# Optimization experiments

Hardware: AMD Instinct MI355X
Metric: run time of the kernel (lower is better)

## Reference

```python
import jax, jax.numpy as jnp
import numpy as np

B, M, DM = 8, 1024, 1024
H, DH, R = 16, 64, 32
DFF, R1, R2, RO = 4096, 512, 512, 512
EPS = 1e-12


def layernorm(x, g, b):
    mu = jnp.mean(x, axis=-1, keepdims=True)
    var = jnp.mean(jnp.square(x - mu), axis=-1, keepdims=True)
    return (x - mu) * jax.lax.rsqrt(var + EPS) * g + b


def setup_inputs() -> dict:
    key = jax.random.key(0)
    ks = jax.random.split(key, 24)
    s = lambda *sh: 1.0 / np.sqrt(sh[-2] if len(sh) > 1 else sh[-1])
    d = {}
    d['x'] = jax.random.normal(ks[0], (B, M, DM), jnp.float32)
    d['mask'] = jnp.zeros((B, M), jnp.float32)  # additive attention mask
    # per-head low-rank QKV factors: P:(H,DM,R), V:(H,R,DH), b:(H,DH)
    for i, nm in enumerate(['q', 'k', 'v']):
        d['P' + nm] = jax.random.normal(ks[1 + 3 * i], (H, DM, R), jnp.float32) * 0.02
        d['V' + nm] = jax.random.normal(ks[2 + 3 * i], (H, R, DH), jnp.float32) * 0.02
        d['b' + nm] = jnp.zeros((H, DH), jnp.float32)
    # attention output projection (low-rank) + LN1
    d['Uo'] = jax.random.normal(ks[10], (DM, RO), jnp.float32) * 0.02
    d['Vo'] = jax.random.normal(ks[11], (RO, DM), jnp.float32) * 0.02
    d['bo_attn'] = jnp.zeros((DM,), jnp.float32)
    d['g1'] = jnp.ones((DM,), jnp.float32)
    d['beta1'] = jnp.zeros((DM,), jnp.float32)
    # FFN low-rank factors + LN2
    d['U1'] = jax.random.normal(ks[12], (DM, R1), jnp.float32) * 0.02
    d['V1'] = jax.random.normal(ks[13], (R1, DFF), jnp.float32) * 0.02
    d['b1'] = jnp.zeros((DFF,), jnp.float32)
    d['U2'] = jax.random.normal(ks[14], (DFF, R2), jnp.float32) * 0.02
    d['V2'] = jax.random.normal(ks[15], (R2, DM), jnp.float32) * 0.02
    d['b2'] = jnp.zeros((DM,), jnp.float32)
    d['g2'] = jnp.ones((DM,), jnp.float32)
    d['beta2'] = jnp.zeros((DM,), jnp.float32)
    return d


def reference(x, mask, Pq, Vq, bq, Pk, Vk, bk, Pv, Vv, bv,
              Uo, Vo, bo_attn, g1, beta1,
              U1, V1, b1, U2, V2, b2, g2, beta2):
    # low-rank Q/K/V: x @ P -> (B,H,M,R), then @ V -> (B,H,M,DH), + bias
    def qkv(P, V, b):
        tmp = jnp.einsum('bmd,hdr->bhmr', x, P)
        return jnp.einsum('bhmr,hre->bhme', tmp, V) + b[None, :, None, :]

    Q = qkv(Pq, Vq, bq)
    K = qkv(Pk, Vk, bk)
    V = qkv(Pv, Vv, bv)
    scale = 1.0 / jnp.sqrt(jnp.asarray(DH, x.dtype))
    scores = jnp.einsum('bhme,bhne->bhmn', Q, K) * scale
    scores = scores + mask[:, None, None, :]  # additive mask broadcast over heads/queries
    probs = jax.nn.softmax(scores, axis=-1)
    attn = jnp.einsum('bhmn,bhne->bhme', probs, V)  # (B,H,M,DH)
    attn = attn.transpose(0, 2, 1, 3).reshape(attn.shape[0], attn.shape[2], -1)  # (B,M,DM)
    x1 = layernorm(x + (attn @ Uo) @ Vo + bo_attn, g1, beta1)
    # FFN: GELU((x1 @ U1) @ V1 + b1) @ U2 @ V2 + b2 (flashsvd_ffn semantics)
    mid = x1 @ U1
    hidden = jax.nn.gelu(mid @ V1 + b1, approximate=False)
    y = (hidden @ U2) @ V2 + b2
    return layernorm(x1 + y, g2, beta2)
```

## Files before the change

### kernel.cpp

```cpp
#include <hip/hip_runtime.h>
#include <hip/hip_bf16.h>
#include <math.h>

typedef unsigned short u16;
typedef unsigned int u32;
typedef __attribute__((ext_vector_type(8))) short bf16x8;
typedef __attribute__((ext_vector_type(4))) float f32x4;
typedef __attribute__((ext_vector_type(2))) unsigned int u32x2;
typedef __attribute__((ext_vector_type(4))) unsigned int u32x4;

#define B_ 8
#define M_ 1024
#define DM_ 1024
#define H_ 16
#define DH_ 64
#define NR_ 8192

__device__ __forceinline__ u16 f2bf(float f) {
    unsigned u = __float_as_uint(f);
    u += 0x7FFFu + ((u >> 16) & 1u);
    return (u16)(u >> 16);
}

__device__ __forceinline__ void gload16(const void* g, void* l) {
    __builtin_amdgcn_global_load_lds(
        (const __attribute__((address_space(1))) void*)g,
        (__attribute__((address_space(3))) void*)l, 16, 0, 0);
}

__device__ __forceinline__ u32 lds_addr(const void* p) {
    return (u32)(uintptr_t)(const __attribute__((address_space(3))) void*)p;
}

__device__ void conv_dev(const float* __restrict__ in, u16* __restrict__ out,
                         int bid, int tid) {
#pragma unroll
    for (int j = 0; j < 4; ++j) {
        int i = bid * 4096 + j * 1024 + tid * 4;
        float4 v = *reinterpret_cast<const float4*>(in + i);
        unsigned long long p = (unsigned long long)f2bf(v.x)
                             | ((unsigned long long)f2bf(v.y) << 16)
                             | ((unsigned long long)f2bf(v.z) << 32)
                             | ((unsigned long long)f2bf(v.w) << 48);
        *reinterpret_cast<unsigned long long*>(out + i) = p;
    }
}

__device__ void prep_p_dev(const float* __restrict__ P, u16* __restrict__ Pt,
                           int h, int kc, int tid, float* sm) {
    float (*Ps)[33] = (float(*)[33])sm;
#pragma unroll
    for (int i = 0; i < 16; ++i) {
        int e = tid + i * 256;
        int kk = e >> 5, r = e & 31;
        Ps[kk][r] = P[(size_t)h * 32768 + (size_t)(kc + kk) * 32 + r];
    }
    __syncthreads();
#pragma unroll
    for (int i = 0; i < 16; ++i) {
        int e = tid + i * 256;
        int r = e >> 7, k = e & 127;
        Pt[(size_t)(h * 32 + r) * 1024 + kc + k] = f2bf(Ps[k][r]);
    }
}

__device__ void prep_f_dev(const float* __restrict__ V, u16* __restrict__ Ft,
                           int h, int tid, float* sm) {
    float (*Vs)[65] = (float(*)[65])sm;
#pragma unroll
    for (int i = 0; i < 8; ++i) {
        int e = tid + i * 256;
        int r = e >> 6, c = e & 63;
        Vs[r][c] = V[(size_t)h * 2048 + r * 64 + c];
    }
    __syncthreads();
#pragma unroll
    for (int i = 0; i < 8; ++i) {
        int idx = tid + i * 256;
        int e = idx >> 5, r = idx & 31;
        Ft[(size_t)h * 2560 + e * 40 + r] = f2bf(Vs[r][e]);
    }
}

__device__ void transp_dev(const float* __restrict__ in, u16* __restrict__ out,
                           int R, int C, int bx, int by, int tid, float* sm) {
    float (*t)[65] = (float(*)[65])sm;
    const int rb = by * 64, cb = bx * 64;
#pragma unroll
    for (int i = 0; i < 16; ++i) {
        int e = tid + i * 256;
        int r = e >> 6, c = e & 63;
        t[r][c] = in[(size_t)(rb + r) * C + cb + c];
    }
    __syncthreads();
#pragma unroll
    for (int i = 0; i < 16; ++i) {
        int e = tid + i * 256;
        int r = e >> 6, c = e & 63;
        out[(size_t)(cb + r) * R + rb + c] = f2bf(t[c][r]);
    }
}

__global__ __launch_bounds__(256) void prep_all(
    const float* __restrict__ x,
    const float* __restrict__ Pq, const float* __restrict__ Pk, const float* __restrict__ Pv,
    const float* __restrict__ Vq, const float* __restrict__ Vk, const float* __restrict__ Vv,
    const float* __restrict__ Uo, const float* __restrict__ Vo,
    const float* __restrict__ U1, const float* __restrict__ V1,
    const float* __restrict__ U2, const float* __restrict__ V2,
    u16* __restrict__ Xb, u16* __restrict__ Pt,
    u16* __restrict__ Ftq, u16* __restrict__ Ftk, u16* __restrict__ Ftv,
    u16* __restrict__ Uot, u16* __restrict__ Vot,
    u16* __restrict__ U1t, u16* __restrict__ V1t,
    u16* __restrict__ U2t, u16* __restrict__ V2t) {
    __shared__ float smem[4224];
    const int bid = blockIdx.x, tid = threadIdx.x;
    if (bid < 2048) {
        conv_dev(x, Xb, bid, tid);
    } else if (bid < 2432) {
        int t = bid - 2048, which = t >> 7, tt = t & 127;
        const float* P = which == 0 ? Pq : (which == 1 ? Pk : Pv);
        prep_p_dev(P, Pt + (size_t)which * 524288, tt >> 3, (tt & 7) * 128, tid, smem);
    } else if (bid < 2480) {
        int t = bid - 2432, which = t >> 4;
        const float* V = which == 0 ? Vq : (which == 1 ? Vk : Vv);
        u16* F = which == 0 ? Ftq : (which == 1 ? Ftk : Ftv);
        prep_f_dev(V, F, t & 15, tid, smem);
    } else if (bid < 2608) {
        int t = bid - 2480;
        transp_dev(Uo, Uot, 1024, 512, t & 7, t >> 3, tid, smem);
    } else if (bid < 2736) {
        int t = bid - 2608;
        transp_dev(Vo, Vot, 512, 1024, t & 15, t >> 4, tid, smem);
    } else if (bid < 2864) {
        int t = bid - 2736;
        transp_dev(U1, U1t, 1024, 512, t & 7, t >> 3, tid, smem);
    } else if (bid < 3376) {
        int t = bid - 2864;
        transp_dev(V1, V1t, 512, 4096, t & 63, t >> 6, tid, smem);
    } else if (bid < 3888) {
        int t = bid - 3376;
        transp_dev(U2, U2t, 4096, 512, t & 7, t >> 3, tid, smem);
    } else {
        int t = bid - 3888;
        transp_dev(V2, V2t, 512, 1024, t & 15, t >> 4, tid, smem);
    }
}

template <int EPI, int NF>
__global__ __launch_bounds__(256) void gemm_bf16(const u16* __restrict__ A,
                                                 const u16* __restrict__ Bt,
                                                 const float* __restrict__ bias,
                                                 void* __restrict__ Cout,
                                                 int K, int N) {
    constexpr int BN = NF * 32;
    __shared__ u16 As[128 * 64];
    __shared__ u16 Bs[BN * 64];
    const int tid = threadIdx.x;
    const int lane = tid & 63, wv = tid >> 6;

    const int NX = gridDim.x;
    const int flat = blockIdx.x + blockIdx.y * NX;
    const int q = (NX * gridDim.y) >> 3;
    const int nid = (flat & 7) * q + (flat >> 3);
    const int row0 = (nid / NX) * 128, col0 = (nid % NX) * BN;

    const int frow = lane & 15, fk8 = lane >> 4;
    const int wm = (wv >> 1) * 64, wn = (wv & 1) * (BN / 2);

    f32x4 acc[4][NF];
    const f32x4 z4 = {0.f, 0.f, 0.f, 0.f};
#pragma unroll
    for (int i = 0; i < 4; ++i)
#pragma unroll
        for (int j = 0; j < NF; ++j) acc[i][j] = z4;

    for (int k0 = 0; k0 < K; k0 += 64) {
#pragma unroll
        for (int i = 0; i < 4; ++i) {
            int rr = (i * 4 + wv) * 8 + (lane >> 3);
            int cc = ((lane & 7) ^ (rr & 7)) * 8;
            gload16(A + (size_t)(row0 + rr) * K + k0 + cc,
                    (char*)As + (i * 4 + wv) * 1024);
        }
#pragma unroll
        for (int i = 0; i < NF; ++i) {
            int rr = (i * 4 + wv) * 8 + (lane >> 3);
            int cc = ((lane & 7) ^ (rr & 7)) * 8;
            gload16(Bt + (size_t)(col0 + rr) * K + k0 + cc,
                    (char*)Bs + (i * 4 + wv) * 1024);
        }
        asm volatile("s_waitcnt vmcnt(0)" ::: "memory");
        __syncthreads();
#pragma unroll
        for (int kf = 0; kf < 2; ++kf) {
            bf16x8 af[4], bfr[NF];
#pragma unroll
            for (int mf = 0; mf < 4; ++mf) {
                int r = wm + mf * 16 + frow;
                int c16 = (kf * 4 + fk8) ^ (r & 7);
                af[mf] = *reinterpret_cast<const bf16x8*>((char*)As + r * 128 + c16 * 16);
            }
#pragma unroll
            for (int nf = 0; nf < NF; ++nf) {
                int r = wn + nf * 16 + frow;
                int c16 = (kf * 4 + fk8) ^ (r & 7);
                bfr[nf] = *reinterpret_cast<const bf16x8*>((char*)Bs + r * 128 + c16 * 16);
            }
#pragma unroll
            for (int mf = 0; mf < 4; ++mf)
#pragma unroll
                for (int nf = 0; nf < NF; ++nf)
                    acc[mf][nf] = __builtin_amdgcn_mfma_f32_16x16x32_bf16(
                        af[mf], bfr[nf], acc[mf][nf], 0, 0, 0);
        }
        __syncthreads();
    }

    const int orow = fk8 * 4, ocol = frow;
#pragma unroll
    for (int mf = 0; mf < 4; ++mf)
#pragma unroll
        for (int nf = 0; nf < NF; ++nf)
#pragma unroll
            for (int j = 0; j < 4; ++j) {
                int row = row0 + wm + mf * 16 + orow + j;
                int col = col0 + wn + nf * 16 + ocol;
                float v = acc[mf][nf][j];
                if (EPI == 2) {
                    v += bias[col];
                    v = 0.5f * v * (1.f + erff(v * 0.70710678118f));
                    ((u16*)Cout)[(size_t)row * N + col] = f2bf(v);
                } else if (EPI == 3) {
                    ((float*)Cout)[(size_t)row * N + col] = v;
                } else {
                    ((u16*)Cout)[(size_t)row * N + col] = f2bf(v);
                }
            }
}

__global__ __launch_bounds__(256) void gemm_db(const u16* __restrict__ A,
                                               const u16* __restrict__ Bt,
                                               u16* __restrict__ Cout,
                                               int K, int N) {
    __shared__ u16 As[2][128 * 64];
    __shared__ u16 Bs[2][64 * 64];
    const int tid = threadIdx.x;
    const int lane = tid & 63, wv = tid >> 6;

    const int NX = gridDim.x;
    const int flat = blockIdx.x + blockIdx.y * NX;
    const int q = (NX * gridDim.y) >> 3;
    const int nid = (flat & 7) * q + (flat >> 3);
    const int row0 = (nid / NX) * 128, col0 = (nid % NX) * 64;

    const int frow = lane & 15, fk8 = lane >> 4;
    const int wm = (wv >> 1) * 64, wn = (wv & 1) * 32;

    f32x4 acc[4][2];
    const f32x4 z4 = {0.f, 0.f, 0.f, 0.f};
#pragma unroll
    for (int i = 0; i < 4; ++i) {
        acc[i][0] = z4;
        acc[i][1] = z4;
    }

    const int srr = (lane >> 3);
    const int scc = (lane & 7);

#pragma unroll
    for (int i = 0; i < 4; ++i) {
        int rr = (i * 4 + wv) * 8 + srr;
        int cc = (scc ^ (rr & 7)) * 8;
        gload16(A + (size_t)(row0 + rr) * K + cc, (char*)&As[0][0] + (i * 4 + wv) * 1024);
    }
#pragma unroll
    for (int i = 0; i < 2; ++i) {
        int rr = (i * 4 + wv) * 8 + srr;
        int cc = (scc ^ (rr & 7)) * 8;
        gload16(Bt + (size_t)(col0 + rr) * K + cc, (char*)&Bs[0][0] + (i * 4 + wv) * 1024);
    }

    int cur = 0;
    for (int k0 = 0; k0 < K; k0 += 64) {
        __syncthreads();
        if (k0 + 64 < K) {
            int kn = k0 + 64;
#pragma unroll
            for (int i = 0; i < 4; ++i) {
                int rr = (i * 4 + wv) * 8 + srr;
                int cc = (scc ^ (rr & 7)) * 8;
                gload16(A + (size_t)(row0 + rr) * K + kn + cc,
                        (char*)&As[cur ^ 1][0] + (i * 4 + wv) * 1024);
            }
#pragma unroll
            for (int i = 0; i < 2; ++i) {
                int rr = (i * 4 + wv) * 8 + srr;
                int cc = (scc ^ (rr & 7)) * 8;
                gload16(Bt + (size_t)(col0 + rr) * K + kn + cc,
                        (char*)&Bs[cur ^ 1][0] + (i * 4 + wv) * 1024);
            }
        }
#pragma unroll
        for (int kf = 0; kf < 2; ++kf) {
            bf16x8 af[4], bfr[2];
#pragma unroll
            for (int mf = 0; mf < 4; ++mf) {
                int r = wm + mf * 16 + frow;
                int c16 = (kf * 4 + fk8) ^ (r & 7);
                af[mf] = *reinterpret_cast<const bf16x8*>((char*)&As[cur][0] + r * 128 + c16 * 16);
            }
#pragma unroll
            for (int nf = 0; nf < 2; ++nf) {
                int r = wn + nf * 16 + frow;
                int c16 = (kf * 4 + fk8) ^ (r & 7);
                bfr[nf] = *reinterpret_cast<const bf16x8*>((char*)&Bs[cur][0] + r * 128 + c16 * 16);
            }
#pragma unroll
            for (int mf = 0; mf < 4; ++mf)
#pragma unroll
                for (int nf = 0; nf < 2; ++nf)
                    acc[mf][nf] = __builtin_amdgcn_mfma_f32_16x16x32_bf16(
                        af[mf], bfr[nf], acc[mf][nf], 0, 0, 0);
        }
        cur ^= 1;
    }

#pragma unroll
    for (int mf = 0; mf < 4; ++mf)
#pragma unroll
        for (int nf = 0; nf < 2; ++nf)
#pragma unroll
            for (int j = 0; j < 4; ++j) {
                int row = row0 + wm + mf * 16 + fk8 * 4 + j;
                int col = col0 + wn + nf * 16 + frow;
                Cout[(size_t)row * N + col] = f2bf(acc[mf][nf][j]);
            }
}

__global__ __launch_bounds__(256) void qkv_s2(const u16* __restrict__ Tmp,
                                              const u16* __restrict__ Ftq,
                                              const u16* __restrict__ Ftk,
                                              const u16* __restrict__ Ftv,
                                              const float* __restrict__ bq,
                                              const float* __restrict__ bk,
                                              const float* __restrict__ bv,
                                              u16* __restrict__ Q,
                                              u16* __restrict__ K,
                                              u16* __restrict__ V) {
    __shared__ u16 Ts[64 * 104];
    const int m0 = blockIdx.x * 64, h = blockIdx.y, tid = threadIdx.x;
    const int lane = tid & 63, wv = tid >> 6;
    const int frow = lane & 15, fk8 = lane >> 4;

    {
        const int row = tid >> 2, seg = tid & 3;
#pragma unroll
        for (int sect = 0; sect < 3; ++sect) {
            int off = sect * 512 + h * 32;
            uint4 v = *reinterpret_cast<const uint4*>(
                Tmp + (size_t)(m0 + row) * 1536 + off + seg * 8);
            *reinterpret_cast<uint4*>(&Ts[row * 104 + sect * 32 + seg * 8]) = v;
        }
    }
    __syncthreads();

    const u16* Fts[3] = {Ftq, Ftk, Ftv};
    const float* bs[3] = {bq, bk, bv};
    u16* outs[3] = {Q, K, V};

    f32x4 acc[3][4];
    const f32x4 z4 = {0.f, 0.f, 0.f, 0.f};
#pragma unroll
    for (int f = 0; f < 3; ++f) {
        bf16x8 a = *reinterpret_cast<const bf16x8*>(
            &Ts[(wv * 16 + frow) * 104 + f * 32 + fk8 * 8]);
#pragma unroll
        for (int nf = 0; nf < 4; ++nf) {
            int e = nf * 16 + frow;
            bf16x8 b = *reinterpret_cast<const bf16x8*>(
                Fts[f] + (size_t)h * 2560 + e * 40 + fk8 * 8);
            acc[f][nf] = __builtin_amdgcn_mfma_f32_16x16x32_bf16(a, b, z4, 0, 0, 0);
        }
    }

    const int bb = m0 >> 10;
#pragma unroll
    for (int f = 0; f < 3; ++f)
#pragma unroll
        for (int nf = 0; nf < 4; ++nf) {
            int e = nf * 16 + frow;
            float bias = bs[f][h * 64 + e];
#pragma unroll
            for (int j = 0; j < 4; ++j) {
                int m = m0 + wv * 16 + fk8 * 4 + j;
                outs[f][(((size_t)(bb * 16 + h) << 10) + (m & 1023)) * 64 + e] =
                    f2bf(acc[f][nf][j] + bias);
            }
        }
}

__global__ __launch_bounds__(256) void attn_mfma(const u16* __restrict__ Q,
                                                 const u16* __restrict__ K,
                                                 const u16* __restrict__ V,
                                                 const float* __restrict__ mask,
                                                 u16* __restrict__ O) {
    __shared__ u16 Ks[4096];
    __shared__ u16 Vt[4096];
    __shared__ u16 Pw[4096];
    const int flat = blockIdx.x;
    const int nid = (flat & 7) * 256 + (flat >> 3);
    const int hb = nid >> 4, qt = nid & 15;
    const int b = hb >> 4, h = hb & 15;
    const int tid = threadIdx.x, lane = tid & 63, wv = tid >> 6;
    const int frow = lane & 15, fk8 = lane >> 4;
    const size_t base = (size_t)hb * 65536;
    const float LOG2E = 1.44269504089f;
    const int srr = lane >> 3, scc = lane & 7;

#pragma unroll
    for (int i = 0; i < 2; ++i) {
        int rr = (i * 4 + wv) * 8 + srr;
        int cc = (scc ^ (rr & 7)) * 8;
        gload16(Q + base + (size_t)(qt * 64 + rr) * 64 + cc,
                (char*)Ks + (i * 4 + wv) * 1024);
    }
    asm volatile("s_waitcnt vmcnt(0)" ::: "memory");
    __syncthreads();
    bf16x8 qfrag[2];
#pragma unroll
    for (int kf = 0; kf < 2; ++kf) {
        int qr = wv * 16 + frow;
        int c16 = (kf * 4 + fk8) ^ (qr & 7);
        qfrag[kf] = *reinterpret_cast<const bf16x8*>((char*)Ks + qr * 128 + c16 * 16);
    }

    int voff[2];
#pragma unroll
    for (int i = 0; i < 2; ++i) {
        int c = (i * 4 + wv) * 64 + lane;
        int kb = c >> 5, db = (c >> 3) & 3, kr = (c >> 1) & 3, hf = c & 1;
        voff[i] = (kb * 4 + kr) * 64 + db * 16 + hf * 8;
    }

    u32 vta[4];
    {
        u32 vt0 = lds_addr(Vt) + fk8 * 1024 + frow * 2;
#pragma unroll
        for (int nf = 0; nf < 4; ++nf) vta[nf] = vt0 + nf * 128;
    }

    char* pwW = (char*)Pw + wv * 2048 + frow * 128 + (fk8 & 1) * 8;
    char* pwR = (char*)Pw + wv * 2048 + frow * 128;
    const float* mrow = mask + b * M_;

    float m_i = -1e30f, l_i = 0.f;
    const f32x4 z4 = {0.f, 0.f, 0.f, 0.f};
    f32x4 o_acc[4] = {z4, z4, z4, z4};

    for (int kt = 0; kt < 16; ++kt) {
        __syncthreads();
#pragma unroll
        for (int i = 0; i < 2; ++i) {
            int rr = (i * 4 + wv) * 8 + srr;
            int cc = (scc ^ (rr & 7)) * 8;
            gload16(K + base + (size_t)(kt * 64 + rr) * 64 + cc,
                    (char*)Ks + (i * 4 + wv) * 1024);
        }
#pragma unroll
        for (int i = 0; i < 2; ++i)
            gload16(V + base + kt * 4096 + voff[i], (char*)Vt + (i * 4 + wv) * 1024);
        asm volatile("s_waitcnt vmcnt(0)" ::: "memory");
        __syncthreads();

        f32x4 sacc[4] = {z4, z4, z4, z4};
        __builtin_amdgcn_s_setprio(1);
#pragma unroll
        for (int kf = 0; kf < 2; ++kf)
#pragma unroll
            for (int nf = 0; nf < 4; ++nf) {
                int kr = nf * 16 + frow;
                int c16 = (kf * 4 + fk8) ^ (kr & 7);
                bf16x8 ak = *reinterpret_cast<const bf16x8*>((char*)Ks + kr * 128 + c16 * 16);
                sacc[nf] = __builtin_amdgcn_mfma_f32_16x16x32_bf16(ak, qfrag[kf], sacc[nf], 0, 0, 0);
            }
        __builtin_amdgcn_s_setprio(0);

        float tval[4][4];
        float tmax = -1e30f;
#pragma unroll
        for (int nf = 0; nf < 4; ++nf) {
            float4 mk = *reinterpret_cast<const float4*>(mrow + kt * 64 + nf * 16 + fk8 * 4);
            float t0 = fmaf(sacc[nf][0], 0.125f, mk.x);
            float t1 = fmaf(sacc[nf][1], 0.125f, mk.y);
            float t2 = fmaf(sacc[nf][2], 0.125f, mk.z);
            float t3 = fmaf(sacc[nf][3], 0.125f, mk.w);
            tval[nf][0] = t0; tval[nf][1] = t1; tval[nf][2] = t2; tval[nf][3] = t3;
            tmax = fmaxf(tmax, fmaxf(fmaxf(t0, t1), fmaxf(t2, t3)));
        }
        tmax = fmaxf(tmax, __shfl_xor(tmax, 16));
        tmax = fmaxf(tmax, __shfl_xor(tmax, 32));

        if (__any(tmax > m_i + 8.f)) {
            float mnew = fmaxf(m_i, tmax);
            float c = exp2f((m_i - mnew) * LOG2E);
            m_i = mnew;
            l_i *= c;
#pragma unroll
            for (int j = 0; j < 4; ++j) {
                float cj = __shfl(c, fk8 * 4 + j);
#pragma unroll
                for (int nf = 0; nf < 4; ++nf) o_acc[nf][j] *= cj;
            }
        }

        const float ml = m_i * LOG2E;
        float rs = 0.f;
#pragma unroll
        for (int nf = 0; nf < 4; ++nf) {
            float p0 = exp2f(fmaf(tval[nf][0], LOG2E, -ml));
            float p1 = exp2f(fmaf(tval[nf][1], LOG2E, -ml));
            float p2 = exp2f(fmaf(tval[nf][2], LOG2E, -ml));
            float p3 = exp2f(fmaf(tval[nf][3], LOG2E, -ml));
            rs += (p0 + p1) + (p2 + p3);
            u32 w0 = __builtin_amdgcn_perm(__float_as_uint(p1), __float_as_uint(p0), 0x07060302u);
            u32 w1 = __builtin_amdgcn_perm(__float_as_uint(p3), __float_as_uint(p2), 0x07060302u);
            u32x2 wp = {w0, w1};
            *reinterpret_cast<u32x2*>(pwW + (((nf * 2 + (fk8 >> 1)) ^ (frow & 7)) * 16)) = wp;
        }
        rs += __shfl_xor(rs, 16);
        rs += __shfl_xor(rs, 32);
        l_i += rs;

#pragma unroll
        for (int kf = 0; kf < 2; ++kf) {
            bf16x8 ap = *reinterpret_cast<const bf16x8*>(pwR + (((kf * 4 + fk8) ^ (frow & 7)) * 16));
            u32x2 r0, r1, r2, r3, r4, r5, r6, r7;
            if (kf == 0) {
                asm volatile("ds_read_b64_tr_b16 %0, %1" : "=&v"(r0) : "v"(vta[0]));
                asm volatile("ds_read_b64_tr_b16 %0, %1 offset:512" : "=&v"(r1) : "v"(vta[0]));
                asm volatile("ds_read_b64_tr_b16 %0, %1" : "=&v"(r2) : "v"(vta[1]));
                asm volatile("ds_read_b64_tr_b16 %0, %1 offset:512" : "=&v"(r3) : "v"(vta[1]));
                asm volatile("ds_read_b64_tr_b16 %0, %1" : "=&v"(r4) : "v"(vta[2]));
                asm volatile("ds_read_b64_tr_b16 %0, %1 offset:512" : "=&v"(r5) : "v"(vta[2]));
                asm volatile("ds_read_b64_tr_b16 %0, %1" : "=&v"(r6) : "v"(vta[3]));
                asm volatile("ds_read_b64_tr_b16 %0, %1 offset:512" : "=&v"(r7) : "v"(vta[3]));
            } else {
                asm volatile("ds_read_b64_tr_b16 %0, %1 offset:4096" : "=&v"(r0) : "v"(vta[0]));
                asm volatile("ds_read_b64_tr_b16 %0, %1 offset:4608" : "=&v"(r1) : "v"(vta[0]));
                asm volatile("ds_read_b64_tr_b16 %0, %1 offset:4096" : "=&v"(r2) : "v"(vta[1]));
                asm volatile("ds_read_b64_tr_b16 %0, %1 offset:4608" : "=&v"(r3) : "v"(vta[1]));
                asm volatile("ds_read_b64_tr_b16 %0, %1 offset:4096" : "=&v"(r4) : "v"(vta[2]));
                asm volatile("ds_read_b64_tr_b16 %0, %1 offset:4608" : "=&v"(r5) : "v"(vta[2]));
                asm volatile("ds_read_b64_tr_b16 %0, %1 offset:4096" : "=&v"(r6) : "v"(vta[3]));
                asm volatile("ds_read_b64_tr_b16 %0, %1 offset:4608" : "=&v"(r7) : "v"(vta[3]));
            }
            asm volatile("s_waitcnt lgkmcnt(0)" ::: "memory");
            __builtin_amdgcn_sched_barrier(0);
            __builtin_amdgcn_s_setprio(1);
            {
                u32x4 vv = {r0.x, r0.y, r1.x, r1.y};
                bf16x8 f; __builtin_memcpy(&f, &vv, 16);
                o_acc[0] = __builtin_amdgcn_mfma_f32_16x16x32_bf16(ap, f, o_acc[0], 0, 0, 0);
            }
            {
                u32x4 vv = {r2.x, r2.y, r3.x, r3.y};
                bf16x8 f; __builtin_memcpy(&f, &vv, 16);
                o_acc[1] = __builtin_amdgcn_mfma_f32_16x16x32_bf16(ap, f, o_acc[1], 0, 0, 0);
            }
            {
                u32x4 vv = {r4.x, r4.y, r5.x, r5.y};
                bf16x8 f; __builtin_memcpy(&f, &vv, 16);
                o_acc[2] = __builtin_amdgcn_mfma_f32_16x16x32_bf16(ap, f, o_acc[2], 0, 0, 0);
            }
            {
                u32x4 vv = {r6.x, r6.y, r7.x, r7.y};
                bf16x8 f; __builtin_memcpy(&f, &vv, 16);
                o_acc[3] = __builtin_amdgcn_mfma_f32_16x16x32_bf16(ap, f, o_acc[3], 0, 0, 0);
            }
            __builtin_amdgcn_s_setprio(0);
        }
    }

#pragma unroll
    for (int j = 0; j < 4; ++j) {
        float lq = __shfl(l_i, fk8 * 4 + j);
        float inv = 1.f / lq;
        int grow = qt * 64 + wv * 16 + fk8 * 4 + j;
        size_t obase = ((size_t)(b * M_ + grow)) * DM_ + h * 64;
#pragma unroll
        for (int nf = 0; nf < 4; ++nf)
            O[obase + nf * 16 + frow] = f2bf(o_acc[nf][j] * inv);
    }
}

template <bool WBF>
__global__ __launch_bounds__(256) void ln_kernel(const float* __restrict__ y,
                                                 const float* __restrict__ res,
                                                 const float* __restrict__ bias,
                                                 const float* __restrict__ g,
                                                 const float* __restrict__ beta,
                                                 float* __restrict__ outf,
                                                 u16* __restrict__ outb) {
    __shared__ float red[2][4];
    const int row = blockIdx.x, tid = threadIdx.x;
    const size_t base = (size_t)row * 1024 + tid * 4;
    float4 v = *reinterpret_cast<const float4*>(y + base);
    float4 r = *reinterpret_cast<const float4*>(res + base);
    float4 bb = *reinterpret_cast<const float4*>(bias + tid * 4);
    v.x += r.x + bb.x; v.y += r.y + bb.y; v.z += r.z + bb.z; v.w += r.w + bb.w;
    float sum = v.x + v.y + v.z + v.w;
    float sq = v.x * v.x + v.y * v.y + v.z * v.z + v.w * v.w;
#pragma unroll
    for (int off = 32; off; off >>= 1) {
        sum += __shfl_down(sum, off);
        sq += __shfl_down(sq, off);
    }
    if ((tid & 63) == 0) { red[0][tid >> 6] = sum; red[1][tid >> 6] = sq; }
    __syncthreads();
    sum = red[0][0] + red[0][1] + red[0][2] + red[0][3];
    sq = red[1][0] + red[1][1] + red[1][2] + red[1][3];
    float mu = sum * (1.f / 1024.f);
    float var = sq * (1.f / 1024.f) - mu * mu;
    float rstd = rsqrtf(var + 1e-12f);
    float4 gg = *reinterpret_cast<const float4*>(g + tid * 4);
    float4 be = *reinterpret_cast<const float4*>(beta + tid * 4);
    float4 o;
    o.x = (v.x - mu) * rstd * gg.x + be.x;
    o.y = (v.y - mu) * rstd * gg.y + be.y;
    o.z = (v.z - mu) * rstd * gg.z + be.z;
    o.w = (v.w - mu) * rstd * gg.w + be.w;
    *reinterpret_cast<float4*>(outf + base) = o;
    if (WBF) {
        unsigned long long p = (unsigned long long)f2bf(o.x)
                             | ((unsigned long long)f2bf(o.y) << 16)
                             | ((unsigned long long)f2bf(o.z) << 32)
                             | ((unsigned long long)f2bf(o.w) << 48);
        *reinterpret_cast<unsigned long long*>(outb + base) = p;
    }
}

extern "C" void kernel_launch(void* const* d_in, const int* in_sizes, int n_in,
                              void* d_out, int out_size, void* d_ws, size_t ws_size,
                              hipStream_t stream) {
    const float* x    = (const float*)d_in[0];
    const float* mask = (const float*)d_in[1];
    const float* Pq   = (const float*)d_in[2];
    const float* Vq   = (const float*)d_in[3];
    const float* bq   = (const float*)d_in[4];
    const float* Pk   = (const float*)d_in[5];
    const float* Vk   = (const float*)d_in[6];
    const float* bk   = (const float*)d_in[7];
    const float* Pv   = (const float*)d_in[8];
    const float* Vv   = (const float*)d_in[9];
    const float* bv   = (const float*)d_in[10];
    const float* Uo   = (const float*)d_in[11];
    const float* Vo   = (const float*)d_in[12];
    const float* bo   = (const float*)d_in[13];
    const float* g1   = (const float*)d_in[14];
    const float* be1  = (const float*)d_in[15];
    const float* U1   = (const float*)d_in[16];
    const float* V1   = (const float*)d_in[17];
    const float* b1   = (const float*)d_in[18];
    const float* U2   = (const float*)d_in[19];
    const float* V2   = (const float*)d_in[20];
    const float* b2   = (const float*)d_in[21];
    const float* g2   = (const float*)d_in[22];
    const float* be2  = (const float*)d_in[23];
    float* out = (float*)d_out;

    const size_t MB = 1048576;
    char* ws = (char*)d_ws;
    u16* Pt  = (u16*)(ws + 0);
    u16* Ftq = (u16*)(ws + 3 * MB);
    u16* Ftk = (u16*)(ws + 3 * MB + 131072);
    u16* Ftv = (u16*)(ws + 3 * MB + 262144);
    u16* Uot = (u16*)(ws + 4 * MB);
    u16* Vot = (u16*)(ws + 5 * MB);
    u16* U1t = (u16*)(ws + 6 * MB);
    u16* V1t = (u16*)(ws + 7 * MB);
    u16* U2t = (u16*)(ws + 11 * MB);
    u16* V2t = (u16*)(ws + 15 * MB);
    u16* Xb  = (u16*)(ws + 16 * MB);
    u16* Tmp = (u16*)(ws + 32 * MB);
    u16* Qb  = (u16*)(ws + 56 * MB);
    u16* Kb  = (u16*)(ws + 72 * MB);
    u16* Vb  = (u16*)(ws + 88 * MB);
    u16* Ob  = (u16*)(ws + 104 * MB);
    u16* Hb  = (u16*)(ws + 32 * MB);
    float* Yf = (float*)(ws + 56 * MB);
    u16* Tb  = (u16*)(ws + 96 * MB);
    float* X1f = (float*)(ws + 120 * MB);

    prep_all<<<4016, 256, 0, stream>>>(x, Pq, Pk, Pv, Vq, Vk, Vv,
                                       Uo, Vo, U1, V1, U2, V2,
                                       Xb, Pt, Ftq, Ftk, Ftv,
                                       Uot, Vot, U1t, V1t, U2t, V2t);

    gemm_bf16<0, 4><<<dim3(12, 64), 256, 0, stream>>>(Xb, Pt, nullptr, Tmp, 1024, 1536);
    qkv_s2<<<dim3(128, 16), 256, 0, stream>>>(Tmp, Ftq, Ftk, Ftv, bq, bk, bv, Qb, Kb, Vb);

    attn_mfma<<<2048, 256, 0, stream>>>(Qb, Kb, Vb, mask, Ob);

    gemm_db<<<dim3(8, 64), 256, 0, stream>>>(Ob, Uot, Tb, 1024, 512);
    gemm_bf16<3, 4><<<dim3(8, 64), 256, 0, stream>>>(Tb, Vot, nullptr, Yf, 512, 1024);
    ln_kernel<true><<<8192, 256, 0, stream>>>(Yf, x, bo, g1, be1, X1f, Xb);

    gemm_db<<<dim3(8, 64), 256, 0, stream>>>(Xb, U1t, Tb, 1024, 512);
    gemm_bf16<2, 4><<<dim3(32, 64), 256, 0, stream>>>(Tb, V1t, b1, Hb, 512, 4096);
    gemm_db<<<dim3(8, 64), 256, 0, stream>>>(Hb, U2t, Tb, 4096, 512);
    gemm_bf16<3, 4><<<dim3(8, 64), 256, 0, stream>>>(Tb, V2t, nullptr, Yf, 512, 1024);
    ln_kernel<false><<<8192, 256, 0, stream>>>(Yf, X1f, b2, g2, be2, out, nullptr);
}
```

Before: 347.5 us.

## Fuse QKV low-rank stages into one GEMM and double-buffer attention K/V tiles

The x@P GEMM and the per-head rank-32 up-projection to Q/K/V become one kernel. The intermediate tile stays in shared memory and is multiplied by the small factor matrices in the epilogue, so the Tmp round-trip through global memory and one launch go away. The attention kernel now double-buffers its K/V tiles, prefetching the next tile while the current one is computed, and stages Q in the P buffer. This uses more shared memory per block, which may lower occupancy, and the fused GEMM uses a larger 128x128 tile that is single-buffered.

```diff
diff --git a/kernel.cpp b/kernel.cpp
--- a/kernel.cpp
+++ b/kernel.cpp
@@ -239,6 +239,127 @@
             }
 }
 
+__global__ __launch_bounds__(256) void gemm_qkv(const u16* __restrict__ A,
+                                                const u16* __restrict__ Bt,
+                                                const u16* __restrict__ Ftq,
+                                                const u16* __restrict__ Ftk,
+                                                const u16* __restrict__ Ftv,
+                                                const float* __restrict__ bq,
+                                                const float* __restrict__ bk,
+                                                const float* __restrict__ bv,
+                                                u16* __restrict__ Qo,
+                                                u16* __restrict__ Ko,
+                                                u16* __restrict__ Vo) {
+    const int K = 1024;
+    __shared__ u16 As[128 * 64];
+    __shared__ u16 Bs[128 * 64];
+    const int tid = threadIdx.x;
+    const int lane = tid & 63, wv = tid >> 6;
+
+    const int NX = gridDim.x;
+    const int flat = blockIdx.x + blockIdx.y * NX;
+    const int q = (NX * gridDim.y) >> 3;
+    const int nid = (flat & 7) * q + (flat >> 3);
+    const int row0 = (nid / NX) * 128, col0 = (nid % NX) * 128;
+
+    const int frow = lane & 15, fk8 = lane >> 4;
+    const int wm = (wv >> 1) * 64, wn = (wv & 1) * 64;
+
+    f32x4 acc[4][4];
+    const f32x4 z4 = {0.f, 0.f, 0.f, 0.f};
+#pragma unroll
+    for (int i = 0; i < 4; ++i)
+#pragma unroll
+        for (int j = 0; j < 4; ++j) acc[i][j] = z4;
+
+    for (int k0 = 0; k0 < K; k0 += 64) {
+#pragma unroll
+        for (int i = 0; i < 4; ++i) {
+            int rr = (i * 4 + wv) * 8 + (lane >> 3);
+            int cc = ((lane & 7) ^ (rr & 7)) * 8;
+            gload16(A + (size_t)(row0 + rr) * K + k0 + cc,
+                    (char*)As + (i * 4 + wv) * 1024);
+            gload16(Bt + (size_t)(col0 + rr) * K + k0 + cc,
+                    (char*)Bs + (i * 4 + wv) * 1024);
+        }
+        asm volatile("s_waitcnt vmcnt(0)" ::: "memory");
+        __syncthreads();
+#pragma unroll
+        for (int kf = 0; kf < 2; ++kf) {
+            bf16x8 af[4], bfr[4];
+#pragma unroll
+            for (int mf = 0; mf < 4; ++mf) {
+                int r = wm + mf * 16 + frow;
+                int c16 = (kf * 4 + fk8) ^ (r & 7);
+                af[mf] = *reinterpret_cast<const bf16x8*>((char*)As + r * 128 + c16 * 16);
+            }
+#pragma unroll
+            for (int nf = 0; nf < 4; ++nf) {
+                int r = wn + nf * 16 + frow;
+                int c16 = (kf * 4 + fk8) ^ (r & 7);
+                bfr[nf] = *reinterpret_cast<const bf16x8*>((char*)Bs + r * 128 + c16 * 16);
+            }
+#pragma unroll
+            for (int mf = 0; mf < 4; ++mf)
+#pragma unroll
+                for (int nf = 0; nf < 4; ++nf)
+                    acc[mf][nf] = __builtin_amdgcn_mfma_f32_16x16x32_bf16(
+                        af[mf], bfr[nf], acc[mf][nf], 0, 0, 0);
+        }
+        __syncthreads();
+    }
+
+    u16* preg = (wv < 2) ? As + wv * 4096 : Bs + (wv - 2) * 4096;
+#pragma unroll
+    for (int mf = 0; mf < 4; ++mf)
+#pragma unroll
+        for (int nf = 0; nf < 4; ++nf)
+#pragma unroll
+            for (int j = 0; j < 4; ++j) {
+                int r = mf * 16 + fk8 * 4 + j;
+                int c = nf * 16 + frow;
+                int byte = r * 128 + (((c >> 3) ^ (r & 7)) * 16) + (c & 7) * 2;
+                *(u16*)((char*)preg + byte) = f2bf(acc[mf][nf][j]);
+            }
+    __syncthreads();
+
+    const int f = col0 >> 9;
+    const u16* Ft = f == 0 ? Ftq : (f == 1 ? Ftk : Ftv);
+    const float* bias = f == 0 ? bq : (f == 1 ? bk : bv);
+    u16* outp = f == 0 ? Qo : (f == 1 ? Ko : Vo);
+    const int h0 = (((col0 & 511) + wn) >> 5);
+
+#pragma unroll
+    for (int hh = 0; hh < 2; ++hh) {
+        const int h = h0 + hh;
+        const u16* ftb = Ft + (size_t)h * 2560;
+        bf16x8 bf2[4];
+#pragma unroll
+        for (int ef = 0; ef < 4; ++ef) {
+            int e = ef * 16 + frow;
+            bf2[ef] = *reinterpret_cast<const bf16x8*>(ftb + e * 40 + fk8 * 8);
+        }
+#pragma unroll
+        for (int mf = 0; mf < 4; ++mf) {
+            int r = mf * 16 + frow;
+            bf16x8 af = *reinterpret_cast<const bf16x8*>(
+                (char*)preg + r * 128 + (((hh * 4 + fk8) ^ (r & 7)) * 16));
+#pragma unroll
+            for (int ef = 0; ef < 4; ++ef) {
+                f32x4 o = __builtin_amdgcn_mfma_f32_16x16x32_bf16(af, bf2[ef], z4, 0, 0, 0);
+                int e = ef * 16 + frow;
+                float bv_ = bias[h * 64 + e];
+#pragma unroll
+                for (int j = 0; j < 4; ++j) {
+                    int row = row0 + wm + mf * 16 + fk8 * 4 + j;
+                    int bb = row >> 10, m = row & 1023;
+                    outp[(((size_t)(bb * 16 + h) << 10) + m) * 64 + e] = f2bf(o[j] + bv_);
+                }
+            }
+        }
+    }
+}
+
 __global__ __launch_bounds__(256) void gemm_db(const u16* __restrict__ A,
                                                const u16* __restrict__ Bt,
                                                u16* __restrict__ Cout,
@@ -338,75 +459,13 @@
             }
 }
 
-__global__ __launch_bounds__(256) void qkv_s2(const u16* __restrict__ Tmp,
-                                              const u16* __restrict__ Ftq,
-                                              const u16* __restrict__ Ftk,
-                                              const u16* __restrict__ Ftv,
-                                              const float* __restrict__ bq,
-                                              const float* __restrict__ bk,
-                                              const float* __restrict__ bv,
-                                              u16* __restrict__ Q,
-                                              u16* __restrict__ K,
-                                              u16* __restrict__ V) {
-    __shared__ u16 Ts[64 * 104];
-    const int m0 = blockIdx.x * 64, h = blockIdx.y, tid = threadIdx.x;
-    const int lane = tid & 63, wv = tid >> 6;
-    const int frow = lane & 15, fk8 = lane >> 4;
-
-    {
-        const int row = tid >> 2, seg = tid & 3;
-#pragma unroll
-        for (int sect = 0; sect < 3; ++sect) {
-            int off = sect * 512 + h * 32;
-            uint4 v = *reinterpret_cast<const uint4*>(
-                Tmp + (size_t)(m0 + row) * 1536 + off + seg * 8);
-            *reinterpret_cast<uint4*>(&Ts[row * 104 + sect * 32 + seg * 8]) = v;
-        }
-    }
-    __syncthreads();
-
-    const u16* Fts[3] = {Ftq, Ftk, Ftv};
-    const float* bs[3] = {bq, bk, bv};
-    u16* outs[3] = {Q, K, V};
-
-    f32x4 acc[3][4];
-    const f32x4 z4 = {0.f, 0.f, 0.f, 0.f};
-#pragma unroll
-    for (int f = 0; f < 3; ++f) {
-        bf16x8 a = *reinterpret_cast<const bf16x8*>(
-            &Ts[(wv * 16 + frow) * 104 + f * 32 + fk8 * 8]);
-#pragma unroll
-        for (int nf = 0; nf < 4; ++nf) {
-            int e = nf * 16 + frow;
-            bf16x8 b = *reinterpret_cast<const bf16x8*>(
-                Fts[f] + (size_t)h * 2560 + e * 40 + fk8 * 8);
-            acc[f][nf] = __builtin_amdgcn_mfma_f32_16x16x32_bf16(a, b, z4, 0, 0, 0);
-        }
-    }
-
-    const int bb = m0 >> 10;
-#pragma unroll
-    for (int f = 0; f < 3; ++f)
-#pragma unroll
-        for (int nf = 0; nf < 4; ++nf) {
-            int e = nf * 16 + frow;
-            float bias = bs[f][h * 64 + e];
-#pragma unroll
-            for (int j = 0; j < 4; ++j) {
-                int m = m0 + wv * 16 + fk8 * 4 + j;
-                outs[f][(((size_t)(bb * 16 + h) << 10) + (m & 1023)) * 64 + e] =
-                    f2bf(acc[f][nf][j] + bias);
-            }
-        }
-}
-
 __global__ __launch_bounds__(256) void attn_mfma(const u16* __restrict__ Q,
                                                  const u16* __restrict__ K,
                                                  const u16* __restrict__ V,
                                                  const float* __restrict__ mask,
                                                  u16* __restrict__ O) {
-    __shared__ u16 Ks[4096];
-    __shared__ u16 Vt[4096];
+    __shared__ u16 Ks[2][4096];
+    __shared__ u16 Vt[2][4096];
     __shared__ u16 Pw[4096];
     const int flat = blockIdx.x;
     const int nid = (flat & 7) * 256 + (flat >> 3);
@@ -418,34 +477,40 @@
     const float LOG2E = 1.44269504089f;
     const int srr = lane >> 3, scc = lane & 7;
 
+    int voff[2];
+#pragma unroll
+    for (int i = 0; i < 2; ++i) {
+        int c = (i * 4 + wv) * 64 + lane;
+        int kb = c >> 5, db = (c >> 3) & 3, kr = (c >> 1) & 3, hf = c & 1;
+        voff[i] = (kb * 4 + kr) * 64 + db * 16 + hf * 8;
+    }
+
 #pragma unroll
     for (int i = 0; i < 2; ++i) {
         int rr = (i * 4 + wv) * 8 + srr;
         int cc = (scc ^ (rr & 7)) * 8;
         gload16(Q + base + (size_t)(qt * 64 + rr) * 64 + cc,
-                (char*)Ks + (i * 4 + wv) * 1024);
-    }
+                (char*)Pw + (i * 4 + wv) * 1024);
+        gload16(K + base + (size_t)rr * 64 + cc,
+                (char*)&Ks[0][0] + (i * 4 + wv) * 1024);
+    }
+#pragma unroll
+    for (int i = 0; i < 2; ++i)
+        gload16(V + base + voff[i], (char*)&Vt[0][0] + (i * 4 + wv) * 1024);
     asm volatile("s_waitcnt vmcnt(0)" ::: "memory");
     __syncthreads();
+
     bf16x8 qfrag[2];
 #pragma unroll
     for (int kf = 0; kf < 2; ++kf) {
         int qr = wv * 16 + frow;
         int c16 = (kf * 4 + fk8) ^ (qr & 7);
-        qfrag[kf] = *reinterpret_cast<const bf16x8*>((char*)Ks + qr * 128 + c16 * 16);
-    }
-
-    int voff[2];
-#pragma unroll
-    for (int i = 0; i < 2; ++i) {
-        int c = (i * 4 + wv) * 64 + lane;
-        int kb = c >> 5, db = (c >> 3) & 3, kr = (c >> 1) & 3, hf = c & 1;
-        voff[i] = (kb * 4 + kr) * 64 + db * 16 + hf * 8;
+        qfrag[kf] = *reinterpret_cast<const bf16x8*>((char*)Pw + qr * 128 + c16 * 16);
     }
 
     u32 vta[4];
     {
-        u32 vt0 = lds_addr(Vt) + fk8 * 1024 + frow * 2;
+        u32 vt0 = lds_addr(&Vt[0][0]) + fk8 * 1024 + frow * 2;
 #pragma unroll
         for (int nf = 0; nf < 4; ++nf) vta[nf] = vt0 + nf * 128;
     }
@@ -458,20 +523,25 @@
     const f32x4 z4 = {0.f, 0.f, 0.f, 0.f};
     f32x4 o_acc[4] = {z4, z4, z4, z4};
 
+    int cur = 0;
     for (int kt = 0; kt < 16; ++kt) {
-        __syncthreads();
-#pragma unroll
-        for (int i = 0; i < 2; ++i) {
-            int rr = (i * 4 + wv) * 8 + srr;
-            int cc = (scc ^ (rr & 7)) * 8;
-            gload16(K + base + (size_t)(kt * 64 + rr) * 64 + cc,
-                    (char*)Ks + (i * 4 + wv) * 1024);
-        }
-#pragma unroll
-        for (int i = 0; i < 2; ++i)
-            gload16(V + base + kt * 4096 + voff[i], (char*)Vt + (i * 4 + wv) * 1024);
-        asm volatile("s_waitcnt vmcnt(0)" ::: "memory");
-        __syncthreads();
+        if (kt < 15) {
+            const int nxt = cur ^ 1;
+#pragma unroll
+            for (int i = 0; i < 2; ++i) {
+                int rr = (i * 4 + wv) * 8 + srr;
+                int cc = (scc ^ (rr & 7)) * 8;
+                gload16(K + base + (kt + 1) * 4096 + (size_t)rr * 64 + cc,
+                        (char*)&Ks[nxt][0] + (i * 4 + wv) * 1024);
+            }
+#pragma unroll
+            for (int i = 0; i < 2; ++i)
+                gload16(V + base + (kt + 1) * 4096 + voff[i],
+                        (char*)&Vt[nxt][0] + (i * 4 + wv) * 1024);
+        }
+
+        const char* ksb = (char*)&Ks[cur][0];
+        const u32 vbo = (u32)(cur * 8192);
 
         f32x4 sacc[4] = {z4, z4, z4, z4};
         __builtin_amdgcn_s_setprio(1);
@@ -481,7 +551,7 @@
             for (int nf = 0; nf < 4; ++nf) {
                 int kr = nf * 16 + frow;
                 int c16 = (kf * 4 + fk8) ^ (kr & 7);
-                bf16x8 ak = *reinterpret_cast<const bf16x8*>((char*)Ks + kr * 128 + c16 * 16);
+                bf16x8 ak = *reinterpret_cast<const bf16x8*>(ksb + kr * 128 + c16 * 16);
                 sacc[nf] = __builtin_amdgcn_mfma_f32_16x16x32_bf16(ak, qfrag[kf], sacc[nf], 0, 0, 0);
             }
         __builtin_amdgcn_s_setprio(0);
@@ -535,51 +605,56 @@
 #pragma unroll
         for (int kf = 0; kf < 2; ++kf) {
             bf16x8 ap = *reinterpret_cast<const bf16x8*>(pwR + (((kf * 4 + fk8) ^ (frow & 7)) * 16));
+            u32 a0 = vta[0] + vbo, a1 = vta[1] + vbo, a2 = vta[2] + vbo, a3 = vta[3] + vbo;
             u32x2 r0, r1, r2, r3, r4, r5, r6, r7;
             if (kf == 0) {
-                asm volatile("ds_read_b64_tr_b16 %0, %1" : "=&v"(r0) : "v"(vta[0]));
-                asm volatile("ds_read_b64_tr_b16 %0, %1 offset:512" : "=&v"(r1) : "v"(vta[0]));
-                asm volatile("ds_read_b64_tr_b16 %0, %1" : "=&v"(r2) : "v"(vta[1]));
-                asm volatile("ds_read_b64_tr_b16 %0, %1 offset:512" : "=&v"(r3) : "v"(vta[1]));
-                asm volatile("ds_read_b64_tr_b16 %0, %1" : "=&v"(r4) : "v"(vta[2]));
-                asm volatile("ds_read_b64_tr_b16 %0, %1 offset:512" : "=&v"(r5) : "v"(vta[2]));
-                asm volatile("ds_read_b64_tr_b16 %0, %1" : "=&v"(r6) : "v"(vta[3]));
-                asm volatile("ds_read_b64_tr_b16 %0, %1 offset:512" : "=&v"(r7) : "v"(vta[3]));
+                asm volatile("ds_read_b64_tr_b16 %0, %1" : "=&v"(r0) : "v"(a0));
+                asm volatile("ds_read_b64_tr_b16 %0, %1 offset:512" : "=&v"(r1) : "v"(a0));
+                asm volatile("ds_read_b64_tr_b16 %0, %1" : "=&v"(r2) : "v"(a1));
+                asm volatile("ds_read_b64_tr_b16 %0, %1 offset:512" : "=&v"(r3) : "v"(a1));
+                asm volatile("ds_read_b64_tr_b16 %0, %1" : "=&v"(r4) : "v"(a2));
+                asm volatile("ds_read_b64_tr_b16 %0, %1 offset:512" : "=&v"(r5) : "v"(a2));
+                asm volatile("ds_read_b64_tr_b16 %0, %1" : "=&v"(r6) : "v"(a3));
+                asm volatile("ds_read_b64_tr_b16 %0, %1 offset:512" : "=&v"(r7) : "v"(a3));
             } else {
-                asm volatile("ds_read_b64_tr_b16 %0, %1 offset:4096" : "=&v"(r0) : "v"(vta[0]));
-                asm volatile("ds_read_b64_tr_b16 %0, %1 offset:4608" : "=&v"(r1) : "v"(vta[0]));
-                asm volatile("ds_read_b64_tr_b16 %0, %1 offset:4096" : "=&v"(r2) : "v"(vta[1]));
-                asm volatile("ds_read_b64_tr_b16 %0, %1 offset:4608" : "=&v"(r3) : "v"(vta[1]));
-                asm volatile("ds_read_b64_tr_b16 %0, %1 offset:4096" : "=&v"(r4) : "v"(vta[2]));
-                asm volatile("ds_read_b64_tr_b16 %0, %1 offset:4608" : "=&v"(r5) : "v"(vta[2]));
-                asm volatile("ds_read_b64_tr_b16 %0, %1 offset:4096" : "=&v"(r6) : "v"(vta[3]));
-                asm volatile("ds_read_b64_tr_b16 %0, %1 offset:4608" : "=&v"(r7) : "v"(vta[3]));
+                asm volatile("ds_read_b64_tr_b16 %0, %1 offset:4096" : "=&v"(r0) : "v"(a0));
+                asm volatile("ds_read_b64_tr_b16 %0, %1 offset:4608" : "=&v"(r1) : "v"(a0));
+                asm volatile("ds_read_b64_tr_b16 %0, %1 offset:4096" : "=&v"(r2) : "v"(a1));
+                asm volatile("ds_read_b64_tr_b16 %0, %1 offset:4608" : "=&v"(r3) : "v"(a1));
+                asm volatile("ds_read_b64_tr_b16 %0, %1 offset:4096" : "=&v"(r4) : "v"(a2));
+                asm volatile("ds_read_b64_tr_b16 %0, %1 offset:4608" : "=&v"(r5) : "v"(a2));
+                asm volatile("ds_read_b64_tr_b16 %0, %1 offset:4096" : "=&v"(r6) : "v"(a3));
+                asm volatile("ds_read_b64_tr_b16 %0, %1 offset:4608" : "=&v"(r7) : "v"(a3));
             }
             asm volatile("s_waitcnt lgkmcnt(0)" ::: "memory");
             __builtin_amdgcn_sched_barrier(0);
             __builtin_amdgcn_s_setprio(1);
             {
                 u32x4 vv = {r0.x, r0.y, r1.x, r1.y};
-                bf16x8 f; __builtin_memcpy(&f, &vv, 16);
-                o_acc[0] = __builtin_amdgcn_mfma_f32_16x16x32_bf16(ap, f, o_acc[0], 0, 0, 0);
+                bf16x8 fb; __builtin_memcpy(&fb, &vv, 16);
+                o_acc[0] = __builtin_amdgcn_mfma_f32_16x16x32_bf16(ap, fb, o_acc[0], 0, 0, 0);
             }
             {
                 u32x4 vv = {r2.x, r2.y, r3.x, r3.y};
-                bf16x8 f; __builtin_memcpy(&f, &vv, 16);
-                o_acc[1] = __builtin_amdgcn_mfma_f32_16x16x32_bf16(ap, f, o_acc[1], 0, 0, 0);
+                bf16x8 fb; __builtin_memcpy(&fb, &vv, 16);
+                o_acc[1] = __builtin_amdgcn_mfma_f32_16x16x32_bf16(ap, fb, o_acc[1], 0, 0, 0);
             }
             {
                 u32x4 vv = {r4.x, r4.y, r5.x, r5.y};
-                bf16x8 f; __builtin_memcpy(&f, &vv, 16);
-                o_acc[2] = __builtin_amdgcn_mfma_f32_16x16x32_bf16(ap, f, o_acc[2], 0, 0, 0);
+                bf16x8 fb; __builtin_memcpy(&fb, &vv, 16);
+                o_acc[2] = __builtin_amdgcn_mfma_f32_16x16x32_bf16(ap, fb, o_acc[2], 0, 0, 0);
             }
             {
                 u32x4 vv = {r6.x, r6.y, r7.x, r7.y};
-                bf16x8 f; __builtin_memcpy(&f, &vv, 16);
-                o_acc[3] = __builtin_amdgcn_mfma_f32_16x16x32_bf16(ap, f, o_acc[3], 0, 0, 0);
+                bf16x8 fb; __builtin_memcpy(&fb, &vv, 16);
+                o_acc[3] = __builtin_amdgcn_mfma_f32_16x16x32_bf16(ap, fb, o_acc[3], 0, 0, 0);
             }
             __builtin_amdgcn_s_setprio(0);
         }
+
+        asm volatile("s_waitcnt vmcnt(0)" ::: "memory");
+        __syncthreads();
+        cur ^= 1;
     }
 
 #pragma unroll
@@ -682,7 +757,6 @@
     u16* U2t = (u16*)(ws + 11 * MB);
     u16* V2t = (u16*)(ws + 15 * MB);
     u16* Xb  = (u16*)(ws + 16 * MB);
-    u16* Tmp = (u16*)(ws + 32 * MB);
     u16* Qb  = (u16*)(ws + 56 * MB);
     u16* Kb  = (u16*)(ws + 72 * MB);
     u16* Vb  = (u16*)(ws + 88 * MB);
@@ -697,8 +771,8 @@
                                        Xb, Pt, Ftq, Ftk, Ftv,
                                        Uot, Vot, U1t, V1t, U2t, V2t);
 
-    gemm_bf16<0, 4><<<dim3(12, 64), 256, 0, stream>>>(Xb, Pt, nullptr, Tmp, 1024, 1536);
-    qkv_s2<<<dim3(128, 16), 256, 0, stream>>>(Tmp, Ftq, Ftk, Ftv, bq, bk, bv, Qb, Kb, Vb);
+    gemm_qkv<<<dim3(12, 64), 256, 0, stream>>>(Xb, Pt, Ftq, Ftk, Ftv,
+                                               bq, bk, bv, Qb, Kb, Vb);
 
     attn_mfma<<<2048, 256, 0, stream>>>(Qb, Kb, Vb, mask, Ob);
 
```

Result: faster. 335.5 us (-3.5%).
